# Kernel tuning notes

Measured on AMD Instinct MI355X. Metric: run time of the kernel, lower is better.

Reference implementation:

```python
import jax, jax.numpy as jnp
import numpy as np

# Config (matches init_kwargs)
B, L, D = 2, 2048, 1024
QH, KVH, HD, FFN = 8, 2, 128, 4096
EPS = 1.1920929e-07  # torch RMSNorm default eps = finfo(float32).eps


def _rope_ts():
    d2 = HD // 2
    freq_exp = (2.0 / HD) * jnp.arange(d2, dtype=jnp.float32)
    return 10000.0 ** freq_exp  # [d2]


def _rope(x):
    # x: [B, L, H, HD], rotated in fp32 (matches x.float() in source)
    d2 = HD // 2
    pos = jnp.arange(L, dtype=jnp.float32)
    rad = pos[:, None] / _rope_ts()[None, :]          # [L, d2]
    s = jnp.sin(rad)[None, :, None, :]                # [1, L, 1, d2]
    c = jnp.cos(rad)[None, :, None, :]
    xf = x.astype(jnp.float32)
    x1, x2 = xf[..., :d2], xf[..., d2:]
    return jnp.concatenate([x1 * c - x2 * s, x2 * c + x1 * s], axis=-1).astype(x.dtype)


def _rmsnorm(x, w):
    xf = x.astype(jnp.float32)
    r = jax.lax.rsqrt(jnp.mean(xf * xf, axis=-1, keepdims=True) + EPS)
    return (xf * r).astype(x.dtype) * w


def setup_inputs() -> dict:
    key = jax.random.key(0)
    ks = jax.random.split(key, 9)
    s = 0.02
    return {
        "x": jax.random.normal(ks[0], (B, L, D), dtype=jnp.float32),
        "ln1_w": jnp.ones((D,), dtype=jnp.float32),
        "wq": jax.random.normal(ks[1], (D, QH * HD), dtype=jnp.float32) * s,
        "wk": jax.random.normal(ks[2], (D, KVH * HD), dtype=jnp.float32) * s,
        "wv": jax.random.normal(ks[3], (D, KVH * HD), dtype=jnp.float32) * s,
        "wo": jax.random.normal(ks[4], (QH * HD, D), dtype=jnp.float32) * s,
        "ln2_w": jnp.ones((D,), dtype=jnp.float32),
        "wg": jax.random.normal(ks[5], (D, FFN), dtype=jnp.float32) * s,
        "wu": jax.random.normal(ks[6], (D, FFN), dtype=jnp.float32) * s,
        "wd": jax.random.normal(ks[7], (FFN, D), dtype=jnp.float32) * s,
    }


def reference(x, ln1_w, wq, wk, wv, wo, ln2_w, wg, wu, wd):
    residual = x
    h = _rmsnorm(x, ln1_w)

    q = _rope((h @ wq).reshape(B, L, QH, HD))          # [B,L,QH,HD]
    k = _rope((h @ wk).reshape(B, L, KVH, HD))         # [B,L,KVH,HD]
    v = (h @ wv).reshape(B, L, KVH, HD)

    rep = QH // KVH  # kv_map = floor(arange(QH)*KVH/QH) == repeat each kv head `rep` times
    qh = jnp.transpose(q, (0, 2, 1, 3)).astype(jnp.float32)                       # [B,QH,L,HD]
    kh = jnp.transpose(jnp.repeat(k, rep, axis=2), (0, 2, 1, 3)).astype(jnp.float32)
    vh = jnp.transpose(jnp.repeat(v, rep, axis=2), (0, 2, 1, 3)).astype(jnp.float32)

    scores = jnp.einsum("bhqd,bhkd->bhqk", qh, kh) / jnp.sqrt(jnp.float32(HD))    # [B,QH,L,L]
    causal = jnp.triu(jnp.ones((L, L), dtype=bool), 1)
    scores = jnp.where(causal, -jnp.inf, scores)
    attn = jax.nn.softmax(scores, axis=-1)
    ctx = jnp.einsum("bhqk,bhkd->bhqd", attn, vh)                                 # [B,QH,L,HD]
    ctx = jnp.transpose(ctx, (0, 2, 1, 3)).reshape(B, L, QH * HD).astype(x.dtype)

    x = ctx @ wo + residual
    residual = x
    h = _rmsnorm(x, ln2_w)
    return (jax.nn.silu(h @ wg) * (h @ wu)) @ wd + residual
```

## Files before the change

kernel.cpp:

```cpp
#include <hip/hip_runtime.h>
#include <hip/hip_bf16.h>
#include <math.h>

#define B_ 2
#define L_ 2048
#define D_ 1024
#define QH_ 8
#define KVH_ 2
#define HD_ 128
#define FFN_ 4096
#define T_ (B_ * L_)
#define EPS_ 1.1920929e-07f

typedef __bf16 bf16x8 __attribute__((ext_vector_type(8)));
typedef float floatx4 __attribute__((ext_vector_type(4)));
typedef unsigned short ushortx8 __attribute__((ext_vector_type(8)));
typedef unsigned short ushortx4 __attribute__((ext_vector_type(4)));

__device__ __forceinline__ unsigned short f2bf(float f) {
  union { float f; unsigned int u; } v;
  v.f = f;
  unsigned int r = v.u + 0x7FFFu + ((v.u >> 16) & 1u);
  return (unsigned short)(r >> 16);
}
__device__ __forceinline__ float bf2f(unsigned short u) {
  union { unsigned int u; float f; } v;
  v.u = ((unsigned int)u) << 16;
  return v.f;
}
__device__ __forceinline__ void gload_lds16(const void* g, void* l) {
  __builtin_amdgcn_global_load_lds((const __attribute__((address_space(1))) void*)g,
                                   (__attribute__((address_space(3))) void*)l, 16, 0, 0);
}

__device__ __forceinline__ void strip_tc(const float* __restrict__ in,
                                         unsigned short* __restrict__ out,
                                         int K, int N, int n0, int k0) {
  __shared__ float tile[4][32][33];
  int t = threadIdx.x;
  int tx = t & 31, ty = t >> 5;
#pragma unroll
  for (int s = 0; s < 4; s++)
#pragma unroll
    for (int r0 = 0; r0 < 4; r0++) {
      int r = ty + r0 * 8;
      tile[s][r][tx] = in[(size_t)(k0 + s * 32 + r) * N + n0 + tx];
    }
  __syncthreads();
  int nr = t >> 3, kq = t & 7;
#pragma unroll
  for (int s = 0; s < 4; s++) {
    ushortx4 o4;
#pragma unroll
    for (int j = 0; j < 4; j++) o4[j] = f2bf(tile[s][kq * 4 + j][nr]);
    *(ushortx4*)(out + (size_t)(n0 + nr) * K + k0 + s * 32 + kq * 4) = o4;
  }
}

__device__ __forceinline__ void rmsnorm_row(const float* __restrict__ x,
                                            const float* __restrict__ w,
                                            unsigned short* __restrict__ o, int row) {
  __shared__ float red[4];
  int t = threadIdx.x;
  const float* xr = x + (size_t)row * D_;
  float4 xv = *(const float4*)(xr + t * 4);
  float ss = xv.x * xv.x + xv.y * xv.y + xv.z * xv.z + xv.w * xv.w;
#pragma unroll
  for (int off = 32; off >= 1; off >>= 1) ss += __shfl_xor(ss, off);
  if ((t & 63) == 0) red[t >> 6] = ss;
  __syncthreads();
  float total = red[0] + red[1] + red[2] + red[3];
  float r = rsqrtf(total * (1.0f / (float)D_) + EPS_);
  float4 wv = *(const float4*)(w + t * 4);
  unsigned short* op = o + (size_t)row * D_ + t * 4;
  op[0] = f2bf(xv.x * r * wv.x);
  op[1] = f2bf(xv.y * r * wv.y);
  op[2] = f2bf(xv.z * r * wv.z);
  op[3] = f2bf(xv.w * r * wv.w);
}

__global__ __launch_bounds__(256) void prep_all(
    const float* __restrict__ wq, const float* __restrict__ wk,
    const float* __restrict__ wv, const float* __restrict__ wo,
    const float* __restrict__ wg, const float* __restrict__ wu,
    const float* __restrict__ wd, unsigned short* __restrict__ wT,
    const float* __restrict__ x, const float* __restrict__ ln1w,
    unsigned short* __restrict__ h_bf) {
  int bid = blockIdx.x;
  if (bid < 3712) {
    const float* in;
    unsigned short* out;
    int K, N, nt, base;
    if (bid < 256)       { in = wq; out = wT;            K = 1024; N = 1024; nt = 32;  base = 0; }
    else if (bid < 320)  { in = wk; out = wT + 1048576;  K = 1024; N = 256;  nt = 8;   base = 256; }
    else if (bid < 384)  { in = wv; out = wT + 1310720;  K = 1024; N = 256;  nt = 8;   base = 320; }
    else if (bid < 640)  { in = wo; out = wT + 1572864;  K = 1024; N = 1024; nt = 32;  base = 384; }
    else if (bid < 1664) { in = wg; out = wT + 2621440;  K = 1024; N = 4096; nt = 128; base = 640; }
    else if (bid < 2688) { in = wu; out = wT + 6815744;  K = 1024; N = 4096; nt = 128; base = 1664; }
    else                 { in = wd; out = wT + 11010048; K = 4096; N = 1024; nt = 32;  base = 2688; }
    int idx = bid - base;
    strip_tc(in, out, K, N, (idx % nt) * 32, (idx / nt) * 128);
  } else {
    rmsnorm_row(x, ln1w, h_bf, bid - 3712);
  }
}

__global__ __launch_bounds__(256) void rmsnorm_bf16_kernel(const float* __restrict__ x,
                                                           const float* __restrict__ w,
                                                           unsigned short* __restrict__ o) {
  rmsnorm_row(x, w, o, blockIdx.x);
}

template <int EPI, int KH>
__global__ __launch_bounds__(256, 3) void gemm_bf16(const unsigned short* __restrict__ A,
                                                    const unsigned short* __restrict__ BT,
                                                    const float* __restrict__ R,
                                                    float* __restrict__ C,
                                                    int M, int N, int K) {
  __shared__ unsigned short As[KH][64 * 32];
  __shared__ unsigned short Bs[KH][128 * 32];
  int t = threadIdx.x;
  int lane = t & 63, wave = t >> 6;
  int m0 = blockIdx.y * 64, n0 = blockIdx.x * 128;

  int row_a = t >> 2;
  int kc = ((t & 3) ^ ((t >> 3) & 3)) * 8;
  const unsigned short* ga0 = A + (size_t)(m0 + row_a) * K + kc;
  const unsigned short* gb0 = BT + (size_t)(n0 + row_a) * K + kc;
  const unsigned short* gb1 = BT + (size_t)(n0 + 64 + row_a) * K + kc;

  int wm = (wave & 1) * 32, wn = (wave >> 1) * 64;
  int fr = lane & 15, quad = lane >> 4;
  int sw = (quad ^ ((fr >> 1) & 3)) * 8;

  floatx4 acc[2][4];
#pragma unroll
  for (int i = 0; i < 2; i++)
#pragma unroll
    for (int j = 0; j < 4; j++) acc[i][j] = (floatx4){0.f, 0.f, 0.f, 0.f};

  for (int k0 = 0; k0 < K; k0 += 32 * KH) {
#pragma unroll
    for (int h = 0; h < KH; h++) {
      int ko = k0 + h * 32;
      gload_lds16(ga0 + ko, As[h] + wave * 512);
      gload_lds16(gb0 + ko, Bs[h] + wave * 512);
      gload_lds16(gb1 + ko, Bs[h] + 2048 + wave * 512);
    }
    __syncthreads();
#pragma unroll
    for (int h = 0; h < KH; h++) {
      const unsigned short* arp = As[h] + (size_t)(wm + fr) * 32 + sw;
      const unsigned short* brp = Bs[h] + (size_t)(wn + fr) * 32 + sw;
      bf16x8 af[2], bfr[4];
#pragma unroll
      for (int i = 0; i < 2; i++)
        af[i] = __builtin_bit_cast(bf16x8, *(const ushortx8*)(arp + i * 16 * 32));
#pragma unroll
      for (int j = 0; j < 4; j++)
        bfr[j] = __builtin_bit_cast(bf16x8, *(const ushortx8*)(brp + j * 16 * 32));
#pragma unroll
      for (int i = 0; i < 2; i++)
#pragma unroll
        for (int j = 0; j < 4; j++)
          acc[i][j] = __builtin_amdgcn_mfma_f32_16x16x32_bf16(af[i], bfr[j], acc[i][j], 0, 0, 0);
    }
    __syncthreads();
  }

  int orow = m0 + wm + quad * 4;
  int ocol = n0 + wn + fr;
#pragma unroll
  for (int i = 0; i < 2; i++) {
#pragma unroll
    for (int r = 0; r < 4; r++) {
      int row = orow + i * 16 + r;
#pragma unroll
      for (int j = 0; j < 4; j++) {
        size_t idx = (size_t)row * N + ocol + j * 16;
        float v = acc[i][j][r];
        if (EPI == 1) C[idx] = v + R[idx];
        else C[idx] = v + C[idx];
      }
    }
  }
}

__global__ __launch_bounds__(256) void gemm_qkv(const unsigned short* __restrict__ A,
                                                const unsigned short* __restrict__ BT,
                                                unsigned short* __restrict__ qb,
                                                unsigned short* __restrict__ Kb,
                                                unsigned short* __restrict__ Vt) {
  constexpr int K = 1024;
  __shared__ unsigned short smem[24576];
  int t = threadIdx.x;
  int lane = t & 63, wave = t >> 6;
  int bx = blockIdx.x;
  int m0 = blockIdx.y * 64, n0 = bx * 128;

  int row_a = t >> 2;
  int kc = ((t & 3) ^ ((t >> 3) & 3)) * 8;
  const unsigned short* ga0 = A + (size_t)(m0 + row_a) * K + kc;
  const unsigned short* gb0 = BT + (size_t)(n0 + row_a) * K + kc;
  const unsigned short* gb1 = BT + (size_t)(n0 + 64 + row_a) * K + kc;

  int wm = (wave & 1) * 32, wn = (wave >> 1) * 64;
  int fr = lane & 15, quad = lane >> 4;
  int sw = (quad ^ ((fr >> 1) & 3)) * 8;

  floatx4 acc[2][4];
#pragma unroll
  for (int i = 0; i < 2; i++)
#pragma unroll
    for (int j = 0; j < 4; j++) acc[i][j] = (floatx4){0.f, 0.f, 0.f, 0.f};

  for (int k0 = 0; k0 < K; k0 += 128) {
#pragma unroll
    for (int h = 0; h < 4; h++) {
      int ko = k0 + h * 32;
      gload_lds16(ga0 + ko, smem + h * 2048 + wave * 512);
      gload_lds16(gb0 + ko, smem + 8192 + h * 4096 + wave * 512);
      gload_lds16(gb1 + ko, smem + 8192 + h * 4096 + 2048 + wave * 512);
    }
    __syncthreads();
#pragma unroll
    for (int h = 0; h < 4; h++) {
      const unsigned short* arp = smem + h * 2048 + (size_t)(wm + fr) * 32 + sw;
      const unsigned short* brp = smem + 8192 + h * 4096 + (size_t)(wn + fr) * 32 + sw;
      bf16x8 af[2], bfr[4];
#pragma unroll
      for (int i = 0; i < 2; i++)
        af[i] = __builtin_bit_cast(bf16x8, *(const ushortx8*)(arp + i * 16 * 32));
#pragma unroll
      for (int j = 0; j < 4; j++)
        bfr[j] = __builtin_bit_cast(bf16x8, *(const ushortx8*)(brp + j * 16 * 32));
#pragma unroll
      for (int i = 0; i < 2; i++)
#pragma unroll
        for (int j = 0; j < 4; j++)
          acc[i][j] = __builtin_amdgcn_mfma_f32_16x16x32_bf16(af[i], bfr[j], acc[i][j], 0, 0, 0);
    }
    __syncthreads();
  }

  unsigned short* scr = smem;
#pragma unroll
  for (int i = 0; i < 2; i++)
#pragma unroll
    for (int r = 0; r < 4; r++)
#pragma unroll
      for (int j = 0; j < 4; j++)
        scr[(size_t)(wm + quad * 4 + i * 16 + r) * 136 + wn + fr + j * 16] =
            f2bf(acc[i][j][r]);
  __syncthreads();

  if (bx < 10) {
    int row = t >> 2, dq = (t & 3) * 16;
    int tok = m0 + row, pos = tok & (L_ - 1), b = tok >> 11;
    float scale_ = (bx < 8) ? 0.08838834764831843f : 1.0f;
    unsigned short lo[16], hi[16];
#pragma unroll
    for (int m = 0; m < 16; m++) {
      int d2 = dq + m;
      float x1 = bf2f(scr[(size_t)row * 136 + d2]);
      float x2 = bf2f(scr[(size_t)row * 136 + d2 + 64]);
      float inv_ts = expf(-0.14391156831f * (float)d2);
      float rad = (float)pos * inv_ts;
      float s = sinf(rad), c = cosf(rad);
      lo[m] = f2bf((x1 * c - x2 * s) * scale_);
      hi[m] = f2bf((x2 * c + x1 * s) * scale_);
    }
    if (bx < 8) {
      unsigned short* dst = qb + (size_t)tok * 1024 + bx * 128;
      *(ushortx8*)(dst + dq) = *(const ushortx8*)(lo);
      *(ushortx8*)(dst + dq + 8) = *(const ushortx8*)(lo + 8);
      *(ushortx8*)(dst + 64 + dq) = *(const ushortx8*)(hi);
      *(ushortx8*)(dst + 64 + dq + 8) = *(const ushortx8*)(hi + 8);
    } else {
      int kvh = bx - 8, bk = b * KVH_ + kvh, swk = pos & 15;
      unsigned short* dst = Kb + ((size_t)bk * L_ + pos) * HD_;
      int c0 = dq >> 3;
      *(ushortx8*)(dst + ((c0) ^ swk) * 8) = *(const ushortx8*)(lo);
      *(ushortx8*)(dst + ((c0 + 1) ^ swk) * 8) = *(const ushortx8*)(lo + 8);
      *(ushortx8*)(dst + ((c0 + 8) ^ swk) * 8) = *(const ushortx8*)(hi);
      *(ushortx8*)(dst + ((c0 + 9) ^ swk) * 8) = *(const ushortx8*)(hi + 8);
    }
  } else {
    int kvh = bx - 10;
    int b = m0 >> 11, key0 = m0 & (L_ - 1), bk = b * KVH_ + kvh;
    int hd = t >> 1, half = t & 1;
#pragma unroll
    for (int c = 0; c < 4; c++) {
      int cp = half * 4 + c, kcc = cp ^ (hd & 7);
      ushortx8 ob;
#pragma unroll
      for (int j = 0; j < 8; j++) ob[j] = scr[(size_t)(kcc * 8 + j) * 136 + hd];
      *(ushortx8*)(Vt + ((size_t)bk * HD_ + hd) * L_ + key0 + cp * 8) = ob;
    }
  }
}

__global__ __launch_bounds__(256, 3) void gemm_gateup2(
    const unsigned short* __restrict__ A,
    const unsigned short* __restrict__ BgT,
    const unsigned short* __restrict__ BuT,
    unsigned short* __restrict__ Cb) {
  constexpr int K = 1024;
  __shared__ unsigned short As[2][128 * 32];
  __shared__ unsigned short Bs[2][256 * 32];

  int t = threadIdx.x;
  int lane = t & 63, wave = t >> 6;
  int m0 = blockIdx.y * 128;
  int n0l = blockIdx.x * 128;

  int row_a = t >> 2;
  int kc = ((t & 3) ^ ((t >> 3) & 3)) * 8;
  const unsigned short* ga0 = A + (size_t)(m0 + row_a) * K + kc;
  const unsigned short* ga1 = ga0 + (size_t)64 * K;
  const unsigned short* gb[4];
#pragma unroll
  for (int q = 0; q < 4; q++) {
    int rb = q * 64 + row_a;
    const unsigned short* src = ((rb & 31) < 16) ? BgT : BuT;
    gb[q] = src + (size_t)(n0l + (rb >> 5) * 16 + (rb & 15)) * K + kc;
  }

  int fr = lane & 15, quad = lane >> 4;
  int sw = (quad ^ ((fr >> 1) & 3)) * 8;
  int wn = wave;

  floatx4 acc[8][4];
#pragma unroll
  for (int i = 0; i < 8; i++)
#pragma unroll
    for (int j = 0; j < 4; j++) acc[i][j] = (floatx4){0.f, 0.f, 0.f, 0.f};

  for (int k0 = 0; k0 < K; k0 += 64) {
#pragma unroll
    for (int h = 0; h < 2; h++) {
      int ko = k0 + h * 32;
      gload_lds16(ga0 + ko, As[h] + wave * 512);
      gload_lds16(ga1 + ko, As[h] + 2048 + wave * 512);
      gload_lds16(gb[0] + ko, Bs[h] + wave * 512);
      gload_lds16(gb[1] + ko, Bs[h] + 2048 + wave * 512);
      gload_lds16(gb[2] + ko, Bs[h] + 4096 + wave * 512);
      gload_lds16(gb[3] + ko, Bs[h] + 6144 + wave * 512);
    }
    __syncthreads();
#pragma unroll
    for (int h = 0; h < 2; h++) {
      const unsigned short* asr = As[h];
      const unsigned short* bsr = Bs[h] + wn * 64 * 32;
      bf16x8 af[8], bfr[4];
#pragma unroll
      for (int j = 0; j < 4; j++)
        bfr[j] = __builtin_bit_cast(
            bf16x8, *(const ushortx8*)(bsr + (size_t)(j * 16 + fr) * 32 + sw));
#pragma unroll
      for (int i = 0; i < 8; i++)
        af[i] = __builtin_bit_cast(
            bf16x8, *(const ushortx8*)(asr + (size_t)(i * 16 + fr) * 32 + sw));
#pragma unroll
      for (int i = 0; i < 8; i++)
#pragma unroll
        for (int j = 0; j < 4; j++)
          acc[i][j] = __builtin_amdgcn_mfma_f32_16x16x32_bf16(af[i], bfr[j],
                                                              acc[i][j], 0, 0, 0);
    }
    __syncthreads();
  }

#pragma unroll
  for (int i = 0; i < 8; i++) {
    int row = m0 + i * 16 + quad * 4;
#pragma unroll
    for (int r = 0; r < 4; r++) {
#pragma unroll
      for (int jj = 0; jj < 2; jj++) {
        float g = acc[i][2 * jj][r];
        float u = acc[i][2 * jj + 1][r];
        int colL = n0l + (wn * 2 + jj) * 16 + fr;
        Cb[(size_t)(row + r) * FFN_ + colL] = f2bf(g / (1.f + __expf(-g)) * u);
      }
    }
  }
}

__global__ __launch_bounds__(256) void attn_mfma(const unsigned short* __restrict__ qb,
                                                 const unsigned short* __restrict__ Kb,
                                                 const unsigned short* __restrict__ Vt,
                                                 unsigned short* __restrict__ ctx) {
  __shared__ unsigned short Ks[64 * 128];
  __shared__ unsigned short Vs[128 * 64];
  __shared__ unsigned short Ps[4][16 * 72];
  int id = blockIdx.x;
  int bh = id & 15;
  int p_ = id >> 4;
  int qt = (p_ < 16) ? p_ : 47 - p_;
  int b = bh >> 3, h = bh & 7;
  int bk = b * KVH_ + (h >> 2);
  int q0 = qt * 64;
  int t = threadIdx.x, lane = t & 63, w = t >> 6;
  int fr = lane & 15, quad = lane >> 4;

  int pos = q0 + w * 16 + fr;
  const unsigned short* qrow = qb + (size_t)(b * L_ + pos) * 1024 + h * HD_;
  bf16x8 qf[4];
#pragma unroll
  for (int kb = 0; kb < 4; kb++)
    qf[kb] = __builtin_bit_cast(bf16x8, *(const ushortx8*)(qrow + kb * 32 + quad * 8));

  floatx4 o_acc[8];
#pragma unroll
  for (int nt = 0; nt < 8; nt++) o_acc[nt] = (floatx4){0.f, 0.f, 0.f, 0.f};
  float l_r[4] = {0.f, 0.f, 0.f, 0.f};
  unsigned short* Psw = Ps[w];
  const unsigned short* kgb = Kb + (size_t)bk * L_ * HD_;
  const unsigned short* vgb = Vt + (size_t)bk * HD_ * L_;
  int rowg0 = q0 + w * 16 + quad * 4;

  for (int kt = 0; kt <= qt; kt++) {
    int kstart = kt * 64;
    bool diag = (kt == qt);
    __syncthreads();
    const unsigned short* ksrc = kgb + (size_t)kstart * HD_;
#pragma unroll
    for (int it = 0; it < 4; it++) {
      int sl = it * 4 + w;
      gload_lds16(ksrc + sl * 512 + lane * 8, Ks + sl * 512);
    }
#pragma unroll
    for (int it = 0; it < 4; it++) {
      int sl = it * 4 + w;
      gload_lds16(vgb + (size_t)(sl * 8 + (lane >> 3)) * L_ + kstart + (lane & 7) * 8,
                  Vs + sl * 512);
    }
    __syncthreads();

    floatx4 s_acc[4];
#pragma unroll
    for (int jt = 0; jt < 4; jt++) s_acc[jt] = (floatx4){0.f, 0.f, 0.f, 0.f};
#pragma unroll
    for (int kb = 0; kb < 4; kb++) {
#pragma unroll
      for (int jt = 0; jt < 4; jt++) {
        bf16x8 kf = __builtin_bit_cast(
            bf16x8, *(const ushortx8*)(Ks + (jt * 16 + fr) * 128 +
                                       (((kb * 4 + quad) ^ fr) * 8)));
        s_acc[jt] = __builtin_amdgcn_mfma_f32_16x16x32_bf16(qf[kb], kf, s_acc[jt], 0, 0, 0);
      }
    }

#pragma unroll
    for (int jt = 0; jt < 4; jt++) {
#pragma unroll
      for (int r = 0; r < 4; r++) {
        float pp;
        if (diag) {
          int keyg = kstart + jt * 16 + fr;
          pp = (keyg <= rowg0 + r) ? __expf(s_acc[jt][r]) : 0.f;
        } else {
          pp = __expf(s_acc[jt][r]);
        }
        l_r[r] += pp;
        Psw[(quad * 4 + r) * 72 + jt * 16 + fr] = f2bf(pp);
      }
    }
    bf16x8 pf0 = __builtin_bit_cast(bf16x8, *(const ushortx8*)(Psw + fr * 72 + quad * 8));
    bf16x8 pf1 =
        __builtin_bit_cast(bf16x8, *(const ushortx8*)(Psw + fr * 72 + 32 + quad * 8));
#pragma unroll
    for (int nt = 0; nt < 8; nt++) {
      bf16x8 vf0 = __builtin_bit_cast(
          bf16x8,
          *(const ushortx8*)(Vs + (nt * 16 + fr) * 64 + ((quad ^ (fr & 7)) * 8)));
      bf16x8 vf1 = __builtin_bit_cast(
          bf16x8,
          *(const ushortx8*)(Vs + (nt * 16 + fr) * 64 + (((4 + quad) ^ (fr & 7)) * 8)));
      o_acc[nt] = __builtin_amdgcn_mfma_f32_16x16x32_bf16(pf0, vf0, o_acc[nt], 0, 0, 0);
      o_acc[nt] = __builtin_amdgcn_mfma_f32_16x16x32_bf16(pf1, vf1, o_acc[nt], 0, 0, 0);
    }
  }

#pragma unroll
  for (int r = 0; r < 4; r++) {
    l_r[r] += __shfl_xor(l_r[r], 1);
    l_r[r] += __shfl_xor(l_r[r], 2);
    l_r[r] += __shfl_xor(l_r[r], 4);
    l_r[r] += __shfl_xor(l_r[r], 8);
  }

  unsigned short* ob =
      ctx + (size_t)(b * L_ + q0 + w * 16 + quad * 4) * 1024 + h * HD_ + fr;
#pragma unroll
  for (int r = 0; r < 4; r++) {
    float inv = 1.f / l_r[r];
    unsigned short* orow = ob + (size_t)r * 1024;
#pragma unroll
    for (int nt = 0; nt < 8; nt++) orow[nt * 16] = f2bf(o_acc[nt][r] * inv);
  }
}

extern "C" void kernel_launch(void* const* d_in, const int* in_sizes, int n_in,
                              void* d_out, int out_size, void* d_ws, size_t ws_size,
                              hipStream_t stream) {
  const float* x    = (const float*)d_in[0];
  const float* ln1w = (const float*)d_in[1];
  const float* wq   = (const float*)d_in[2];
  const float* wk   = (const float*)d_in[3];
  const float* wvp  = (const float*)d_in[4];
  const float* wo   = (const float*)d_in[5];
  const float* ln2w = (const float*)d_in[6];
  const float* wg   = (const float*)d_in[7];
  const float* wu   = (const float*)d_in[8];
  const float* wd   = (const float*)d_in[9];
  float* out = (float*)d_out;
  char* ws = (char*)d_ws;

  unsigned short* wT = (unsigned short*)ws;
  unsigned short* wqkvT = wT;
  unsigned short* woT = wT + 1572864;
  unsigned short* wgT = wT + 2621440;
  unsigned short* wuT = wT + 6815744;
  unsigned short* wdT = wT + 11010048;
  unsigned short* h_bf = (unsigned short*)(ws + 30408704);
  unsigned short* qb = (unsigned short*)(ws + 38797312);
  unsigned short* h2_bf = (unsigned short*)(ws + 51380224);
  unsigned short* Kb = (unsigned short*)(ws + 59768832);
  unsigned short* Vt = (unsigned short*)(ws + 61865984);
  unsigned short* gu = (unsigned short*)(ws + 59768832);
  unsigned short* ctx_bf = h_bf;

  dim3 blk(256);

  prep_all<<<3712 + T_, blk, 0, stream>>>(wq, wk, wvp, wo, wg, wu, wd, wT, x, ln1w, h_bf);
  gemm_qkv<<<dim3(12, 64), blk, 0, stream>>>(h_bf, wqkvT, qb, Kb, Vt);
  attn_mfma<<<512, blk, 0, stream>>>(qb, Kb, Vt, ctx_bf);
  gemm_bf16<1, 4><<<dim3(8, 64), blk, 0, stream>>>(ctx_bf, woT, x, out, T_, 1024, 1024);
  rmsnorm_bf16_kernel<<<T_, blk, 0, stream>>>(out, ln2w, h2_bf);
  gemm_gateup2<<<dim3(32, 32), blk, 0, stream>>>(h2_bf, wgT, wuT, gu);
  gemm_bf16<2, 4><<<dim3(8, 64), blk, 0, stream>>>(gu, wdT, nullptr, out, T_, 1024, FFN_);
}
```

Baseline: 371.7 us.

## Rewrite gate/up GEMM as 8-wave ping-pong pipelined kernel with 256-row tiles

```diff
diff --git a/kernel.cpp b/kernel.cpp
--- a/kernel.cpp
+++ b/kernel.cpp
@@ -300,35 +300,38 @@
   }
 }
 
-__global__ __launch_bounds__(256, 3) void gemm_gateup2(
+__global__ __launch_bounds__(512, 1) void gemm_gateup8p(
     const unsigned short* __restrict__ A,
     const unsigned short* __restrict__ BgT,
     const unsigned short* __restrict__ BuT,
     unsigned short* __restrict__ Cb) {
   constexpr int K = 1024;
-  __shared__ unsigned short As[2][128 * 32];
-  __shared__ unsigned short Bs[2][256 * 32];
+  __shared__ unsigned short As[2][2][8192];
+  __shared__ unsigned short Bs[2][2][8192];
 
   int t = threadIdx.x;
   int lane = t & 63, wave = t >> 6;
-  int m0 = blockIdx.y * 128;
+  int m0 = blockIdx.y * 256;
   int n0l = blockIdx.x * 128;
 
-  int row_a = t >> 2;
+  int row_s = t >> 2;
   int kc = ((t & 3) ^ ((t >> 3) & 3)) * 8;
-  const unsigned short* ga0 = A + (size_t)(m0 + row_a) * K + kc;
-  const unsigned short* ga1 = ga0 + (size_t)64 * K;
-  const unsigned short* gb[4];
-#pragma unroll
-  for (int q = 0; q < 4; q++) {
-    int rb = q * 64 + row_a;
+  const unsigned short* gaB[2];
+  gaB[0] = A + (size_t)(m0 + row_s) * K + kc;
+  gaB[1] = A + (size_t)(m0 + 128 + row_s) * K + kc;
+  const unsigned short* gbB[2];
+#pragma unroll
+  for (int hf = 0; hf < 2; hf++) {
+    int rb = hf * 128 + row_s;
     const unsigned short* src = ((rb & 31) < 16) ? BgT : BuT;
-    gb[q] = src + (size_t)(n0l + (rb >> 5) * 16 + (rb & 15)) * K + kc;
-  }
-
+    gbB[hf] = src + (size_t)(n0l + (rb >> 5) * 16 + (rb & 15)) * K + kc;
+  }
+
+  int wm = wave >> 2, wn = wave & 3;
   int fr = lane & 15, quad = lane >> 4;
   int sw = (quad ^ ((fr >> 1) & 3)) * 8;
-  int wn = wave;
+  int aro = (wm * 128 + fr) * 32 + sw;
+  int bro = (wn * 64 + fr) * 32 + sw;
 
   floatx4 acc[8][4];
 #pragma unroll
@@ -336,44 +339,104 @@
 #pragma unroll
     for (int j = 0; j < 4; j++) acc[i][j] = (floatx4){0.f, 0.f, 0.f, 0.f};
 
-  for (int k0 = 0; k0 < K; k0 += 64) {
-#pragma unroll
-    for (int h = 0; h < 2; h++) {
-      int ko = k0 + h * 32;
-      gload_lds16(ga0 + ko, As[h] + wave * 512);
-      gload_lds16(ga1 + ko, As[h] + 2048 + wave * 512);
-      gload_lds16(gb[0] + ko, Bs[h] + wave * 512);
-      gload_lds16(gb[1] + ko, Bs[h] + 2048 + wave * 512);
-      gload_lds16(gb[2] + ko, Bs[h] + 4096 + wave * 512);
-      gload_lds16(gb[3] + ko, Bs[h] + 6144 + wave * 512);
-    }
-    __syncthreads();
-#pragma unroll
-    for (int h = 0; h < 2; h++) {
-      const unsigned short* asr = As[h];
-      const unsigned short* bsr = Bs[h] + wn * 64 * 32;
-      bf16x8 af[8], bfr[4];
-#pragma unroll
-      for (int j = 0; j < 4; j++)
-        bfr[j] = __builtin_bit_cast(
-            bf16x8, *(const ushortx8*)(bsr + (size_t)(j * 16 + fr) * 32 + sw));
-#pragma unroll
-      for (int i = 0; i < 8; i++)
-        af[i] = __builtin_bit_cast(
-            bf16x8, *(const ushortx8*)(asr + (size_t)(i * 16 + fr) * 32 + sw));
-#pragma unroll
-      for (int i = 0; i < 8; i++)
-#pragma unroll
-        for (int j = 0; j < 4; j++)
-          acc[i][j] = __builtin_amdgcn_mfma_f32_16x16x32_bf16(af[i], bfr[j],
-                                                              acc[i][j], 0, 0, 0);
-    }
-    __syncthreads();
-  }
+  bf16x8 af[4][2], b0[2][2], b1[2][2];
+
+#define GU_LDA(buf_, ilo_)                                                        \
+  { _Pragma("unroll") for (int i_ = 0; i_ < 4; i_++) {                            \
+      af[i_][0] = __builtin_bit_cast(                                             \
+          bf16x8, *(const ushortx8*)(&As[buf_][0][aro + ((ilo_) + i_) * 512]));   \
+      af[i_][1] = __builtin_bit_cast(                                             \
+          bf16x8, *(const ushortx8*)(&As[buf_][1][aro + ((ilo_) + i_) * 512])); } }
+
+#define GU_LDB(buf_, jlo_, bp_)                                                   \
+  { _Pragma("unroll") for (int j_ = 0; j_ < 2; j_++) {                            \
+      bp_[j_][0] = __builtin_bit_cast(                                            \
+          bf16x8, *(const ushortx8*)(&Bs[buf_][0][bro + ((jlo_) + j_) * 512]));   \
+      bp_[j_][1] = __builtin_bit_cast(                                            \
+          bf16x8, *(const ushortx8*)(&Bs[buf_][1][bro + ((jlo_) + j_) * 512])); } }
+
+#define GU_MM(ilo_, jlo_, bp_)                                                    \
+  { __builtin_amdgcn_s_setprio(1);                                                \
+    _Pragma("unroll") for (int i_ = 0; i_ < 4; i_++)                              \
+        _Pragma("unroll") for (int j_ = 0; j_ < 2; j_++) {                        \
+      acc[(ilo_) + i_][(jlo_) + j_] = __builtin_amdgcn_mfma_f32_16x16x32_bf16(    \
+          af[i_][0], bp_[j_][0], acc[(ilo_) + i_][(jlo_) + j_], 0, 0, 0);         \
+      acc[(ilo_) + i_][(jlo_) + j_] = __builtin_amdgcn_mfma_f32_16x16x32_bf16(    \
+          af[i_][1], bp_[j_][1], acc[(ilo_) + i_][(jlo_) + j_], 0, 0, 0); }       \
+    __builtin_amdgcn_s_setprio(0); }
+
+#define GU_STA(buf_, tile_, half_)                                                \
+  { const unsigned short* g_ = gaB[half_] + (size_t)(tile_) * 64;                 \
+    gload_lds16(g_, &As[buf_][0][(half_) * 4096 + wave * 512]);                   \
+    gload_lds16(g_ + 32, &As[buf_][1][(half_) * 4096 + wave * 512]); }
+
+#define GU_STB(buf_, tile_, half_)                                                \
+  { const unsigned short* g_ = gbB[half_] + (size_t)(tile_) * 64;                 \
+    gload_lds16(g_, &Bs[buf_][0][(half_) * 4096 + wave * 512]);                   \
+    gload_lds16(g_ + 32, &Bs[buf_][1][(half_) * 4096 + wave * 512]); }
+
+#define GU_BAR __builtin_amdgcn_s_barrier()
+#define GU_LGKM0 asm volatile("s_waitcnt lgkmcnt(0)" ::: "memory")
+#define GU_VM4 asm volatile("s_waitcnt vmcnt(4)" ::: "memory")
+#define GU_VM0 asm volatile("s_waitcnt vmcnt(0)" ::: "memory")
+
+  GU_STB(0, 0, 0); GU_STB(0, 0, 1);
+  GU_STA(0, 0, 0); GU_STA(0, 0, 1);
+  GU_STB(1, 1, 0); GU_STB(1, 1, 1);
+  GU_VM4;
+  GU_BAR;
+
+#pragma unroll 1
+  for (int n = 0; n < 7; n++) {
+    int tb = 2 * n + 1, t2 = 2 * n + 2, t3 = 2 * n + 3;
+    GU_LDA(0, 0); GU_LDB(0, 0, b0); GU_STA(1, tb, 0);
+    GU_BAR; GU_LGKM0; GU_MM(0, 0, b0); GU_BAR;
+    GU_LDB(0, 2, b1); GU_STA(1, tb, 1);
+    GU_BAR; GU_LGKM0; GU_MM(0, 2, b1); GU_BAR;
+    GU_LDA(0, 4); GU_STB(0, t2, 0);
+    GU_BAR; GU_LGKM0; GU_MM(4, 0, b0); GU_BAR;
+    GU_STB(0, t2, 1);
+    GU_VM4;
+    GU_BAR; GU_LGKM0; GU_MM(4, 2, b1); GU_BAR;
+    GU_LDA(1, 0); GU_LDB(1, 0, b0); GU_STA(0, t2, 0);
+    GU_BAR; GU_LGKM0; GU_MM(0, 0, b0); GU_BAR;
+    GU_LDB(1, 2, b1); GU_STA(0, t2, 1);
+    GU_BAR; GU_LGKM0; GU_MM(0, 2, b1); GU_BAR;
+    GU_LDA(1, 4); GU_STB(1, t3, 0);
+    GU_BAR; GU_LGKM0; GU_MM(4, 0, b0); GU_BAR;
+    GU_STB(1, t3, 1);
+    GU_VM4;
+    GU_BAR; GU_LGKM0; GU_MM(4, 2, b1); GU_BAR;
+  }
+  GU_LDA(0, 0); GU_LDB(0, 0, b0); GU_STA(1, 15, 0);
+  GU_BAR; GU_LGKM0; GU_MM(0, 0, b0); GU_BAR;
+  GU_LDB(0, 2, b1); GU_STA(1, 15, 1);
+  GU_BAR; GU_LGKM0; GU_MM(0, 2, b1); GU_BAR;
+  GU_LDA(0, 4);
+  GU_BAR; GU_LGKM0; GU_MM(4, 0, b0); GU_BAR;
+  GU_VM0;
+  GU_BAR; GU_LGKM0; GU_MM(4, 2, b1); GU_BAR;
+  GU_LDA(1, 0); GU_LDB(1, 0, b0);
+  GU_BAR; GU_LGKM0; GU_MM(0, 0, b0); GU_BAR;
+  GU_LDB(1, 2, b1);
+  GU_BAR; GU_LGKM0; GU_MM(0, 2, b1); GU_BAR;
+  GU_LDA(1, 4);
+  GU_BAR; GU_LGKM0; GU_MM(4, 0, b0); GU_BAR;
+  GU_MM(4, 2, b1);
+
+#undef GU_LDA
+#undef GU_LDB
+#undef GU_MM
+#undef GU_STA
+#undef GU_STB
+#undef GU_BAR
+#undef GU_LGKM0
+#undef GU_VM4
+#undef GU_VM0
 
 #pragma unroll
   for (int i = 0; i < 8; i++) {
-    int row = m0 + i * 16 + quad * 4;
+    int row = m0 + wm * 128 + i * 16 + quad * 4;
 #pragma unroll
     for (int r = 0; r < 4; r++) {
 #pragma unroll
@@ -539,6 +602,6 @@
   attn_mfma<<<512, blk, 0, stream>>>(qb, Kb, Vt, ctx_bf);
   gemm_bf16<1, 4><<<dim3(8, 64), blk, 0, stream>>>(ctx_bf, woT, x, out, T_, 1024, 1024);
   rmsnorm_bf16_kernel<<<T_, blk, 0, stream>>>(out, ln2w, h2_bf);
-  gemm_gateup2<<<dim3(32, 32), blk, 0, stream>>>(h2_bf, wgT, wuT, gu);
+  gemm_gateup8p<<<dim3(32, 16), dim3(512), 0, stream>>>(h2_bf, wgT, wuT, gu);
   gemm_bf16<2, 4><<<dim3(8, 64), blk, 0, stream>>>(gu, wdT, nullptr, out, T_, 1024, FFN_);
 }
```

Result: no change. 367.6 us (-1.1%).
